# Optimization experiments

Measured on AMD Instinct MI355X. Metric: run time of the kernel, lower is better.

Reference implementation:

```python
import jax, jax.numpy as jnp
import numpy as np

N_NODES = 100000
N_EDGES = 1600000
N_GRAPHS = 1000
HID = 64
NEG_SLOPE = 0.2


def _glorot(key, shape):
    fan_in, fan_out = shape[0], shape[-1]
    lim = float(np.sqrt(6.0 / (fan_in + fan_out)))
    return jax.random.uniform(key, shape, jnp.float32, -lim, lim)


def setup_inputs() -> dict:
    key = jax.random.key(0)
    ks = jax.random.split(key, 20)
    x = jax.random.normal(ks[0], (N_NODES, 1), jnp.float32)
    edge_index = jax.random.randint(ks[1], (2, N_EDGES), 0, N_NODES, jnp.int64)
    batch = jnp.sort(jax.random.randint(ks[2], (N_NODES,), 0, N_GRAPHS, jnp.int64))
    inp = {"x": x, "edge_index": edge_index, "batch": batch}
    # GATv2Conv layer 1 (in=3 -> out=HID, 1 head)
    inp["Wl1"] = _glorot(ks[3], (3, HID)); inp["bl1"] = jnp.zeros((HID,), jnp.float32)
    inp["Wr1"] = _glorot(ks[4], (3, HID)); inp["br1"] = jnp.zeros((HID,), jnp.float32)
    inp["a1"] = _glorot(ks[5], (HID, 1))[:, 0]; inp["b1"] = jnp.zeros((HID,), jnp.float32)
    # GATv2Conv layer 2 (HID -> HID)
    inp["Wl2"] = _glorot(ks[6], (HID, HID)); inp["bl2"] = jnp.zeros((HID,), jnp.float32)
    inp["Wr2"] = _glorot(ks[7], (HID, HID)); inp["br2"] = jnp.zeros((HID,), jnp.float32)
    inp["a2"] = _glorot(ks[8], (HID, 1))[:, 0]; inp["b2"] = jnp.zeros((HID,), jnp.float32)
    # lin2 (HID -> 2)
    inp["W3"] = _glorot(ks[9], (HID, 2)); inp["b3"] = jnp.zeros((2,), jnp.float32)
    return inp


def gatv2_layer(x, src, dst, Wl, bl, Wr, br, a, b):
    """GATv2Conv, 1 head, add_self_loops=True, negative_slope=0.2."""
    n = x.shape[0]
    xl = x @ Wl + bl  # source-side transform [N, C]
    xr = x @ Wr + br  # target-side transform [N, C]
    loops = jnp.arange(n, dtype=src.dtype)
    s = jnp.concatenate([src, loops])
    d = jnp.concatenate([dst, loops])
    # per-edge attention logit: a^T LeakyReLU(xl[j] + xr[i])
    e = jax.nn.leaky_relu(xl[s] + xr[d], NEG_SLOPE) @ a  # [E+N]
    # segment softmax over incoming edges of each dst node
    m = jax.ops.segment_max(e, d, num_segments=n)
    ex = jnp.exp(e - m[d])
    denom = jax.ops.segment_sum(ex, d, num_segments=n)
    alpha = ex / denom[d]
    out = jax.ops.segment_sum(alpha[:, None] * xl[s], d, num_segments=n)
    return out + b


def reference(x, edge_index, batch, Wl1, bl1, Wr1, br1, a1, b1,
              Wl2, bl2, Wr2, br2, a2, b2, W3, b3):
    n = x.shape[0]
    src, dst = edge_index[0], edge_index[1]
    ones = jnp.ones((src.shape[0],), jnp.float32)
    deg_in = jax.ops.segment_sum(ones, dst, num_segments=n)   # bincount(dst)
    deg_out = jax.ops.segment_sum(ones, src, num_segments=n)  # bincount(src)
    h = jnp.concatenate([x, deg_in[:, None], deg_out[:, None]], axis=1)  # [N,3]
    h = gatv2_layer(h, src, dst, Wl1, bl1, Wr1, br1, a1, b1)
    h = jnp.tanh(h)
    h = gatv2_layer(h, src, dst, Wl2, bl2, Wr2, br2, a2, b2)
    # global_max_pool over graphs
    g = jax.ops.segment_max(h, batch, num_segments=N_GRAPHS)  # [G, HID]
    return g @ W3 + b3  # [G, 2]
```

## Files before the change

### kernel.cpp

```cpp
#include <hip/hip_runtime.h>
#include <hip/hip_bf16.h>
#include <hip/hip_fp16.h>

#define HID 64
#define NEG_SLOPE 0.2f
#define BLK_E 4096
#define EDGE_CAP 6144
#define NDB 16

typedef _Float16 f16x2 __attribute__((ext_vector_type(2)));


__global__ void k_hist2(const int* __restrict__ src, const int* __restrict__ dst,
                        int* __restrict__ histS, int* __restrict__ histD,
                        int E, int NB, int NBLK) {
    __shared__ int hs[512], hd[512];
    int t = threadIdx.x, blk = blockIdx.x;
    for (int b = t; b < NB; b += 1024) { hs[b] = 0; hd[b] = 0; }
    __syncthreads();
    int base = blk * BLK_E;
    #pragma unroll
    for (int k = 0; k < BLK_E / 1024; ++k) {
        int i = base + k * 1024 + t;
        if (i < E) {
            atomicAdd(&hs[src[i] >> 8], 1);
            atomicAdd(&hd[dst[i] >> 8], 1);
        }
    }
    __syncthreads();
    for (int b = t; b < NB; b += 1024) {
        histS[b * NBLK + blk] = hs[b];
        histD[b * NBLK + blk] = hd[b];
    }
}

__global__ void k_binscan(int* __restrict__ histS, int* __restrict__ histD,
                          int* __restrict__ totS, int* __restrict__ totD,
                          int NB, int NBLK) {
    __shared__ int s[512];
    int b = blockIdx.x;
    int* hist = histS; int* tot = totS;
    if (b >= NB) { b -= NB; hist = histD; tot = totD; }
    int t = threadIdx.x;
    int v = (t < NBLK) ? hist[b * NBLK + t] : 0;
    s[t] = v;
    __syncthreads();
    for (int o = 1; o < 512; o <<= 1) {
        int u = (t >= o) ? s[t - o] : 0;
        __syncthreads();
        s[t] += u;
        __syncthreads();
    }
    if (t < NBLK) hist[b * NBLK + t] = s[t] - v;
    if (t == 511) tot[b] = s[511];
}

__global__ void k_binoffset(const int* __restrict__ totS, const int* __restrict__ totD,
                            int* __restrict__ bsS, int* __restrict__ bsD,
                            int NB, int E, int* __restrict__ row_off, int N) {
    __shared__ int s[512];
    int t = threadIdx.x;
    int v = (t < NB) ? totS[t] : 0;
    s[t] = v; __syncthreads();
    for (int o = 1; o < 512; o <<= 1) {
        int u = (t >= o) ? s[t - o] : 0;
        __syncthreads(); s[t] += u; __syncthreads();
    }
    if (t < NB) bsS[t] = s[t] - v;
    if (t == 0) bsS[NB] = E;
    __syncthreads();
    v = (t < NB) ? totD[t] : 0;
    s[t] = v; __syncthreads();
    for (int o = 1; o < 512; o <<= 1) {
        int u = (t >= o) ? s[t - o] : 0;
        __syncthreads(); s[t] += u; __syncthreads();
    }
    if (t < NB) bsD[t] = s[t] - v;
    if (t == 0) { bsD[NB] = E; row_off[N] = E; }
}

__global__ void k_scatter_bins(const int* __restrict__ src, const int* __restrict__ dst,
                               const int* __restrict__ histS, const int* __restrict__ histD,
                               const int* __restrict__ bsS, const int* __restrict__ bsD,
                               unsigned* __restrict__ packS, unsigned* __restrict__ packD,
                               int E, int NB, int NBLK) {
    __shared__ int baseS[512], baseD[512];
    int t = threadIdx.x, blk = blockIdx.x;
    for (int b = t; b < NB; b += 1024) {
        baseS[b] = bsS[b] + histS[b * NBLK + blk];
        baseD[b] = bsD[b] + histD[b * NBLK + blk];
    }
    __syncthreads();
    int base = blk * BLK_E;
    #pragma unroll
    for (int k = 0; k < BLK_E / 1024; ++k) {
        int i = base + k * 1024 + t;
        if (i < E) {
            int sv = src[i], dv = dst[i];
            int pD = atomicAdd(&baseD[dv >> 8], 1);
            packD[pD] = ((unsigned)(dv & 255) << 24) | (unsigned)sv;
            int pS = atomicAdd(&baseS[sv >> 8], 1);
            packS[pS] = (unsigned)(sv & 255);
        }
    }
}

__global__ void k_csr_bin_fused(const unsigned* __restrict__ packD, const int* __restrict__ bsD,
                                const unsigned* __restrict__ packS, const int* __restrict__ bsS,
                                int* __restrict__ row_off, float* __restrict__ deg_in,
                                int* __restrict__ csr_src,
                                const float* __restrict__ x,
                                const float* __restrict__ Wl, const float* __restrict__ bl,
                                const float* __restrict__ Wr, const float* __restrict__ br,
                                __half* __restrict__ A, __half* __restrict__ B, int N) {
    __shared__ int cnt[256], off[256], cur[256], cntS[256];
    __shared__ unsigned eb[EDGE_CAP];
    int b = blockIdx.x, t = threadIdx.x;
    int lo = bsD[b], hi = bsD[b + 1], ne = hi - lo;
    bool fits = (ne <= EDGE_CAP);
    if (t < 256) { cnt[t] = 0; cntS[t] = 0; }
    __syncthreads();
    for (int i = t; i < ne; i += 1024) {
        unsigned v = packD[lo + i];
        if (fits) eb[i] = v;
        atomicAdd(&cnt[v >> 24], 1);
    }
    int loS = bsS[b], hiS = bsS[b + 1];
    for (int i = loS + t; i < hiS; i += 1024) atomicAdd(&cntS[packS[i] & 255], 1);
    __syncthreads();
    if (t < 256) off[t] = cnt[t];
    __syncthreads();
    for (int o = 1; o < 256; o <<= 1) {
        int u = 0;
        if (t < 256 && t >= o) u = off[t - o];
        __syncthreads();
        if (t < 256) off[t] += u;
        __syncthreads();
    }
    if (t < 256) {
        int ex = off[t] - cnt[t];
        cur[t] = lo + ex;
        int node = b * 256 + t;
        if (node < N) {
            row_off[node] = lo + ex;
            deg_in[node] = (float)cnt[t];
        }
    }
    __syncthreads();
    for (int i = t; i < ne; i += 1024) {
        unsigned v = fits ? eb[i] : packD[lo + i];
        int pos = atomicAdd(&cur[v >> 24], 1);
        csr_src[pos] = (int)(v & 0xFFFFFFu);
    }
    int nd = b * 256 + (t >> 2);
    if (nd < N) {
        float h0 = x[nd];
        float h1 = (float)cnt[t >> 2];
        float h2 = (float)cntS[t >> 2];
        int c0 = (t & 3) * 16;
        unsigned ua[4], ub[4];
        #pragma unroll
        for (int p = 0; p < 2; ++p) {
            #pragma unroll
            for (int q = 0; q < 4; ++q) {
                int c = c0 + p * 8 + q * 2;
                float a0 = h0 * Wl[c]     + h1 * Wl[64 + c]     + h2 * Wl[128 + c]     + bl[c];
                float a1 = h0 * Wl[c + 1] + h1 * Wl[64 + c + 1] + h2 * Wl[128 + c + 1] + bl[c + 1];
                float b0 = h0 * Wr[c]     + h1 * Wr[64 + c]     + h2 * Wr[128 + c]     + br[c];
                float b1 = h0 * Wr[c + 1] + h1 * Wr[64 + c + 1] + h2 * Wr[128 + c + 1] + br[c + 1];
                f16x2 pa; pa.x = (_Float16)a0; pa.y = (_Float16)a1;
                f16x2 pb; pb.x = (_Float16)b0; pb.y = (_Float16)b1;
                if (q < 4) { ua[q] = __builtin_bit_cast(unsigned, pa); ub[q] = __builtin_bit_cast(unsigned, pb); }
            }
            uint4 sa = make_uint4(ua[0], ua[1], ua[2], ua[3]);
            uint4 sb = make_uint4(ub[0], ub[1], ub[2], ub[3]);
            ((uint4*)A)[(size_t)nd * 8 + (t & 3) * 2 + p] = sa;
            ((uint4*)B)[(size_t)nd * 8 + (t & 3) * 2 + p] = sb;
        }
    }
}


__global__ void k_deghist(const float* __restrict__ deg_in, int* __restrict__ dhist, int N) {
    __shared__ int h[64];
    int t = threadIdx.x, b = blockIdx.x;
    if (t < 64) h[t] = 0;
    __syncthreads();
    int chunk = (N + NDB - 1) / NDB;
    int lo = b * chunk, hi = lo + chunk; if (hi > N) hi = N;
    for (int i = lo + t; i < hi; i += 1024) {
        int dg = (int)deg_in[i]; if (dg > 63) dg = 63;
        atomicAdd(&h[dg], 1);
    }
    __syncthreads();
    if (t < 64) dhist[t * NDB + b] = h[t];
}

__global__ void k_degscan(int* __restrict__ dhist) {
    __shared__ int s[1024];
    int t = threadIdx.x;
    int v = dhist[t];
    s[t] = v; __syncthreads();
    for (int o = 1; o < 1024; o <<= 1) {
        int u = (t >= o) ? s[t - o] : 0;
        __syncthreads(); s[t] += u; __syncthreads();
    }
    dhist[t] = s[t] - v;
}

__global__ void k_degscatter(const float* __restrict__ deg_in, const int* __restrict__ dhist,
                             int* __restrict__ perm, int N) {
    __shared__ int cur[64];
    int t = threadIdx.x, b = blockIdx.x;
    if (t < 64) cur[t] = dhist[t * NDB + b];
    __syncthreads();
    int chunk = (N + NDB - 1) / NDB;
    int lo = b * chunk, hi = lo + chunk; if (hi > N) hi = N;
    for (int i = lo + t; i < hi; i += 1024) {
        int dg = (int)deg_in[i]; if (dg > 63) dg = 63;
        int p = atomicAdd(&cur[dg], 1);
        perm[p] = i;
    }
}


struct H4 { f16x2 h[4]; };

__device__ __forceinline__ f16x2 bch2(unsigned u) {
    return __builtin_bit_cast(f16x2, u);
}

__device__ __forceinline__ H4 ld4(const uint4* __restrict__ T, size_t idx) {
    uint4 r = T[idx];
    H4 o;
    o.h[0] = bch2(r.x); o.h[1] = bch2(r.y); o.h[2] = bch2(r.z); o.h[3] = bch2(r.w);
    return o;
}

__device__ __forceinline__ float logit8(const H4& a, const H4& x,
                                        const float* __restrict__ awf, f16x2 ns2) {
    float t = 0.0f;
    #pragma unroll
    for (int j = 0; j < 4; ++j) {
        f16x2 s = a.h[j] + x.h[j];
        f16x2 l = __builtin_elementwise_max(s, ns2 * s);
        t = fmaf((float)l.x, awf[2 * j], t);
        t = fmaf((float)l.y, awf[2 * j + 1], t);
    }
    return t;
}

__device__ __forceinline__ void accum8(float* __restrict__ acc, const H4& a, float w) {
    #pragma unroll
    for (int j = 0; j < 4; ++j) {
        acc[2 * j]     = fmaf((float)a.h[j].x, w, acc[2 * j]);
        acc[2 * j + 1] = fmaf((float)a.h[j].y, w, acc[2 * j + 1]);
    }
}

template <typename OUT, bool TANH>
__global__ void k_gat_fused(const int* __restrict__ csr_src, const int* __restrict__ row_off,
                            const int* __restrict__ perm,
                            const __half* __restrict__ Ah, const __half* __restrict__ Bh,
                            const float* __restrict__ aw, const float* __restrict__ bias,
                            OUT* __restrict__ out, int N) {
    int tid = blockIdx.x * blockDim.x + threadIdx.x;
    int r = tid >> 3;
    int gl = threadIdx.x & 7;
    if (r >= N) return;
    int d = perm[N - 1 - r];

    const uint4* A16 = (const uint4*)Ah;
    const uint4* B16 = (const uint4*)Bh;
    f16x2 ns2;
    ns2.x = (_Float16)NEG_SLOPE; ns2.y = (_Float16)NEG_SLOPE;

    float awf[8], bw[8];
    {
        const float4* a4 = (const float4*)aw;
        const float4* b4 = (const float4*)bias;
        #pragma unroll
        for (int j = 0; j < 2; ++j) {
            float4 v = a4[gl * 2 + j];
            awf[4 * j] = v.x; awf[4 * j + 1] = v.y; awf[4 * j + 2] = v.z; awf[4 * j + 3] = v.w;
            float4 u = b4[gl * 2 + j];
            bw[4 * j] = u.x; bw[4 * j + 1] = u.y; bw[4 * j + 2] = u.z; bw[4 * j + 3] = u.w;
        }
    }

    size_t rowbase = (size_t)d * 8 + gl;
    H4 xh = ld4(B16, rowbase);
    H4 as = ld4(A16, rowbase);

    float t = logit8(as, xh, awf, ns2);
    t += __shfl_xor(t, 1); t += __shfl_xor(t, 2); t += __shfl_xor(t, 4);
    float m = t, denom = 1.0f;
    float acc[8];
    #pragma unroll
    for (int j = 0; j < 4; ++j) {
        acc[2 * j] = (float)as.h[j].x;
        acc[2 * j + 1] = (float)as.h[j].y;
    }

    int lo = row_off[d], hi = row_off[d + 1];
    int k = lo;
    for (; k + 3 < hi; k += 4) {
        int s0 = csr_src[k], s1 = csr_src[k + 1], s2 = csr_src[k + 2], s3 = csr_src[k + 3];
        H4 a0 = ld4(A16, (size_t)s0 * 8 + gl);
        H4 a1 = ld4(A16, (size_t)s1 * 8 + gl);
        H4 a2 = ld4(A16, (size_t)s2 * 8 + gl);
        H4 a3 = ld4(A16, (size_t)s3 * 8 + gl);
        float t0 = logit8(a0, xh, awf, ns2);
        float t1 = logit8(a1, xh, awf, ns2);
        float t2 = logit8(a2, xh, awf, ns2);
        float t3 = logit8(a3, xh, awf, ns2);
        t0 += __shfl_xor(t0, 1); t1 += __shfl_xor(t1, 1);
        t2 += __shfl_xor(t2, 1); t3 += __shfl_xor(t3, 1);
        t0 += __shfl_xor(t0, 2); t1 += __shfl_xor(t1, 2);
        t2 += __shfl_xor(t2, 2); t3 += __shfl_xor(t3, 2);
        t0 += __shfl_xor(t0, 4); t1 += __shfl_xor(t1, 4);
        t2 += __shfl_xor(t2, 4); t3 += __shfl_xor(t3, 4);
        float mx = fmaxf(fmaxf(t0, t1), fmaxf(t2, t3));
        if (mx > m) {
            float sc = __expf(m - mx);
            denom *= sc;
            #pragma unroll
            for (int j = 0; j < 8; ++j) acc[j] *= sc;
            m = mx;
        }
        float w0 = __expf(t0 - m), w1 = __expf(t1 - m);
        float w2 = __expf(t2 - m), w3 = __expf(t3 - m);
        denom += (w0 + w1) + (w2 + w3);
        accum8(acc, a0, w0);
        accum8(acc, a1, w1);
        accum8(acc, a2, w2);
        accum8(acc, a3, w3);
    }
    for (; k < hi; ++k) {
        int s0 = csr_src[k];
        H4 a0 = ld4(A16, (size_t)s0 * 8 + gl);
        float t0 = logit8(a0, xh, awf, ns2);
        t0 += __shfl_xor(t0, 1); t0 += __shfl_xor(t0, 2); t0 += __shfl_xor(t0, 4);
        if (t0 > m) {
            float sc = __expf(m - t0);
            denom *= sc;
            #pragma unroll
            for (int j = 0; j < 8; ++j) acc[j] *= sc;
            m = t0;
        }
        float w0 = __expf(t0 - m);
        denom += w0;
        accum8(acc, a0, w0);
    }

    float inv = 1.0f / denom;
    float v[8];
    #pragma unroll
    for (int j = 0; j < 8; ++j) {
        v[j] = acc[j] * inv + bw[j];
        if (TANH) v[j] = tanhf(v[j]);
    }
    if constexpr (sizeof(OUT) == 2) {
        unsigned u[4];
        #pragma unroll
        for (int j = 0; j < 4; ++j) {
            f16x2 p; p.x = (_Float16)v[2 * j]; p.y = (_Float16)v[2 * j + 1];
            u[j] = __builtin_bit_cast(unsigned, p);
        }
        ((uint4*)out)[(size_t)d * 8 + gl] = make_uint4(u[0], u[1], u[2], u[3]);
    } else {
        float4* o4 = (float4*)out;
        o4[(size_t)d * 16 + gl * 2]     = make_float4(v[0], v[1], v[2], v[3]);
        o4[(size_t)d * 16 + gl * 2 + 1] = make_float4(v[4], v[5], v[6], v[7]);
    }
}

__global__ __launch_bounds__(512) void k_xfrm2(
        const __half* __restrict__ H,
        const float* __restrict__ Wl, const float* __restrict__ bl,
        const float* __restrict__ Wr, const float* __restrict__ br,
        __half* __restrict__ A, __half* __restrict__ B, int N) {
    __shared__ float wls[4096];
    __shared__ float wrs[4096];
    __shared__ float hst[64 * 66];
    int t = threadIdx.x;
    int base = blockIdx.x * 64;

    ((float4*)wls)[t * 2]     = ((const float4*)Wl)[t * 2];
    ((float4*)wls)[t * 2 + 1] = ((const float4*)Wl)[t * 2 + 1];
    ((float4*)wrs)[t * 2]     = ((const float4*)Wr)[t * 2];
    ((float4*)wrs)[t * 2 + 1] = ((const float4*)Wr)[t * 2 + 1];

    {
        int nd = t >> 3, q = t & 7;
        int node = base + nd;
        uint4 hv = (node < N) ? ((const uint4*)H)[(size_t)node * 8 + q]
                              : make_uint4(0, 0, 0, 0);
        f16x2 p0 = bch2(hv.x), p1 = bch2(hv.y), p2 = bch2(hv.z), p3 = bch2(hv.w);
        int c = q * 8;
        hst[(c + 0) * 66 + nd] = (float)p0.x;
        hst[(c + 1) * 66 + nd] = (float)p0.y;
        hst[(c + 2) * 66 + nd] = (float)p1.x;
        hst[(c + 3) * 66 + nd] = (float)p1.y;
        hst[(c + 4) * 66 + nd] = (float)p2.x;
        hst[(c + 5) * 66 + nd] = (float)p2.y;
        hst[(c + 6) * 66 + nd] = (float)p3.x;
        hst[(c + 7) * 66 + nd] = (float)p3.y;
    }
    __syncthreads();

    int w = t >> 6, l = t & 63;
    float acL[8] = {0, 0, 0, 0, 0, 0, 0, 0};
    float acR[8] = {0, 0, 0, 0, 0, 0, 0, 0};
    #pragma unroll 4
    for (int kk = 0; kk < 64; ++kk) {
        float hv = hst[kk * 66 + l];
        const float4* wl4 = (const float4*)&wls[kk * 64 + w * 8];
        const float4* wr4 = (const float4*)&wrs[kk * 64 + w * 8];
        float4 w0 = wl4[0], w1 = wl4[1];
        float4 r0 = wr4[0], r1 = wr4[1];
        acL[0] = fmaf(hv, w0.x, acL[0]); acL[1] = fmaf(hv, w0.y, acL[1]);
        acL[2] = fmaf(hv, w0.z, acL[2]); acL[3] = fmaf(hv, w0.w, acL[3]);
        acL[4] = fmaf(hv, w1.x, acL[4]); acL[5] = fmaf(hv, w1.y, acL[5]);
        acL[6] = fmaf(hv, w1.z, acL[6]); acL[7] = fmaf(hv, w1.w, acL[7]);
        acR[0] = fmaf(hv, r0.x, acR[0]); acR[1] = fmaf(hv, r0.y, acR[1]);
        acR[2] = fmaf(hv, r0.z, acR[2]); acR[3] = fmaf(hv, r0.w, acR[3]);
        acR[4] = fmaf(hv, r1.x, acR[4]); acR[5] = fmaf(hv, r1.y, acR[5]);
        acR[6] = fmaf(hv, r1.z, acR[6]); acR[7] = fmaf(hv, r1.w, acR[7]);
    }

    int node = base + l;
    if (node < N) {
        float4 bl0 = ((const float4*)bl)[w * 2], bl1 = ((const float4*)bl)[w * 2 + 1];
        float4 br0 = ((const float4*)br)[w * 2], br1 = ((const float4*)br)[w * 2 + 1];
        __half2* A2 = (__half2*)A;
        __half2* B2 = (__half2*)B;
        size_t bo = (size_t)node * 32 + w * 4;
        A2[bo + 0] = __floats2half2_rn(acL[0] + bl0.x, acL[1] + bl0.y);
        A2[bo + 1] = __floats2half2_rn(acL[2] + bl0.z, acL[3] + bl0.w);
        A2[bo + 2] = __floats2half2_rn(acL[4] + bl1.x, acL[5] + bl1.y);
        A2[bo + 3] = __floats2half2_rn(acL[6] + bl1.z, acL[7] + bl1.w);
        B2[bo + 0] = __floats2half2_rn(acR[0] + br0.x, acR[1] + br0.y);
        B2[bo + 1] = __floats2half2_rn(acR[2] + br0.z, acR[3] + br0.w);
        B2[bo + 2] = __floats2half2_rn(acR[4] + br1.x, acR[5] + br1.y);
        B2[bo + 3] = __floats2half2_rn(acR[6] + br1.z, acR[7] + br1.w);
    }
}

__global__ void k_pool_final(const float* __restrict__ C, const float* __restrict__ b2,
                             const int* __restrict__ batch,
                             const float* __restrict__ W3, const float* __restrict__ b3,
                             float* __restrict__ out, int N, int G) {
    int w = (int)((blockIdx.x * (size_t)blockDim.x + threadIdx.x) >> 6);
    int lane = threadIdx.x & 63;
    if (w >= G) return;
    int lo = 0, hi = N;
    while (lo < hi) { int mid = (lo + hi) >> 1; if (batch[mid] < w) lo = mid + 1; else hi = mid; }
    int s0 = lo;
    hi = N;
    while (lo < hi) { int mid = (lo + hi) >> 1; if (batch[mid] < w + 1) lo = mid + 1; else hi = mid; }
    int e0 = lo;

    float acc = -INFINITY;
    int i = s0;
    for (; i + 3 < e0; i += 4) {
        float v0 = C[(size_t)i * HID + lane];
        float v1 = C[(size_t)(i + 1) * HID + lane];
        float v2 = C[(size_t)(i + 2) * HID + lane];
        float v3 = C[(size_t)(i + 3) * HID + lane];
        acc = fmaxf(acc, fmaxf(fmaxf(v0, v1), fmaxf(v2, v3)));
    }
    for (; i < e0; ++i) acc = fmaxf(acc, C[(size_t)i * HID + lane]);
    float v = acc + b2[lane];

    float p0 = v * W3[lane * 2];
    float p1 = v * W3[lane * 2 + 1];
    #pragma unroll
    for (int o = 32; o; o >>= 1) { p0 += __shfl_xor(p0, o); p1 += __shfl_xor(p1, o); }
    if (lane == 0) {
        out[(size_t)w * 2]     = p0 + b3[0];
        out[(size_t)w * 2 + 1] = p1 + b3[1];
    }
}

extern "C" void kernel_launch(void* const* d_in, const int* in_sizes, int n_in,
                              void* d_out, int out_size, void* d_ws, size_t ws_size,
                              hipStream_t stream) {
    const float* x     = (const float*)d_in[0];
    const int*   ei    = (const int*)d_in[1];
    const int*   batch = (const int*)d_in[2];
    const float* Wl1 = (const float*)d_in[3];
    const float* bl1 = (const float*)d_in[4];
    const float* Wr1 = (const float*)d_in[5];
    const float* br1 = (const float*)d_in[6];
    const float* a1  = (const float*)d_in[7];
    const float* b1  = (const float*)d_in[8];
    const float* Wl2 = (const float*)d_in[9];
    const float* bl2 = (const float*)d_in[10];
    const float* Wr2 = (const float*)d_in[11];
    const float* br2 = (const float*)d_in[12];
    const float* a2  = (const float*)d_in[13];
    const float* b2  = (const float*)d_in[14];
    const float* W3  = (const float*)d_in[15];
    const float* b3  = (const float*)d_in[16];

    const int N = in_sizes[0];
    const int E = in_sizes[1] / 2;
    const int G = out_size / 2;
    const int NB = (N + 255) >> 8;
    const int NBLK = (E + BLK_E - 1) / BLK_E;

    float* ws = (float*)d_ws;
    size_t off = 0;
    float*  C  = ws + off; off += (size_t)N * HID;
    __half* Ah = (__half*)(ws + off); off += (size_t)N * HID / 2;
    __half* Bh = (__half*)(ws + off); off += (size_t)N * HID / 2;
    int*   row_off = (int*)(ws + off); off += N + 1;
    int*   csr_src = (int*)(ws + off); off += E;
    float* deg_in  = ws + off; off += N;
    int*   perm    = (int*)(ws + off); off += N;
    int*   dhist   = (int*)(ws + off); off += 1024;
    int*   bsS  = (int*)(ws + off); off += NB + 1;
    int*   bsD  = (int*)(ws + off); off += NB + 1;
    int*   totS = (int*)(ws + off); off += NB;
    int*   totD = (int*)(ws + off); off += NB;

    unsigned* packD = (unsigned*)C;
    unsigned* packS = packD + E;
    int* histS = (int*)(packS + E);
    int* histD = histS + (size_t)NB * NBLK;
    __half* Chalf = (__half*)C;

    const int* src  = ei;
    const int* dstp = ei + E;

    const int BT = 256;
    dim3 blk(BT);
    int grid_g8 = (int)(((size_t)N * 8 + BT - 1) / BT);
    int grid_x2 = (N + 63) / 64;

    k_hist2<<<NBLK, 1024, 0, stream>>>(src, dstp, histS, histD, E, NB, NBLK);
    k_binscan<<<2 * NB, 512, 0, stream>>>(histS, histD, totS, totD, NB, NBLK);
    k_binoffset<<<1, 512, 0, stream>>>(totS, totD, bsS, bsD, NB, E, row_off, N);
    k_scatter_bins<<<NBLK, 1024, 0, stream>>>(src, dstp, histS, histD, bsS, bsD,
                                              packS, packD, E, NB, NBLK);
    k_csr_bin_fused<<<NB, 1024, 0, stream>>>(packD, bsD, packS, bsS, row_off, deg_in,
                                             csr_src, x, Wl1, bl1, Wr1, br1, Ah, Bh, N);

    k_deghist<<<NDB, 1024, 0, stream>>>(deg_in, dhist, N);
    k_degscan<<<1, 1024, 0, stream>>>(dhist);
    k_degscatter<<<NDB, 1024, 0, stream>>>(deg_in, dhist, perm, N);

    k_gat_fused<__half, true><<<grid_g8, blk, 0, stream>>>(csr_src, row_off, perm,
                                                           Ah, Bh, a1, b1, Chalf, N);

    k_xfrm2<<<grid_x2, 512, 0, stream>>>(Chalf, Wl2, bl2, Wr2, br2, Ah, Bh, N);
    k_gat_fused<float, false><<<grid_g8, blk, 0, stream>>>(csr_src, row_off, perm,
                                                           Ah, Bh, a2, b2, C, N);

    k_pool_final<<<(G * 64 + BT - 1) / BT, blk, 0, stream>>>(C, b2, batch, W3, b3,
                                                             (float*)d_out, N, G);
}
```

Measured before the change: 218.1 us.

## Restructure layer-2 transform to one node per thread with register-held features

The layer-2 node transform now assigns one node per thread. Each thread loads its 64-wide half feature row straight into registers instead of transposing it through shared memory, then computes 16 output columns at a time over 8 column blocks. Weights in shared memory are read with wave-uniform broadcast addresses, and the block shrinks to 128 threads. This removes the shared-memory transpose and its bank traffic, but it adds heavy register pressure (64 features plus 16 accumulators), gives each thread strided per-node global loads, and leaves fewer total threads. A redundant always-true guard in the layer-1 packing loop is also dropped.

Result: slower. 225.0 us (+3.1%).

```diff
diff --git a/kernel.cpp b/kernel.cpp
--- a/kernel.cpp
+++ b/kernel.cpp
@@ -170,7 +170,8 @@
                 float b1 = h0 * Wr[c + 1] + h1 * Wr[64 + c + 1] + h2 * Wr[128 + c + 1] + br[c + 1];
                 f16x2 pa; pa.x = (_Float16)a0; pa.y = (_Float16)a1;
                 f16x2 pb; pb.x = (_Float16)b0; pb.y = (_Float16)b1;
-                if (q < 4) { ua[q] = __builtin_bit_cast(unsigned, pa); ub[q] = __builtin_bit_cast(unsigned, pb); }
+                ua[q] = __builtin_bit_cast(unsigned, pa);
+                ub[q] = __builtin_bit_cast(unsigned, pb);
             }
             uint4 sa = make_uint4(ua[0], ua[1], ua[2], ua[3]);
             uint4 sb = make_uint4(ub[0], ub[1], ub[2], ub[3]);
@@ -375,75 +376,73 @@
     }
 }
 
-__global__ __launch_bounds__(512) void k_xfrm2(
+__global__ __launch_bounds__(128) void k_xfrm2(
         const __half* __restrict__ H,
         const float* __restrict__ Wl, const float* __restrict__ bl,
         const float* __restrict__ Wr, const float* __restrict__ br,
         __half* __restrict__ A, __half* __restrict__ B, int N) {
     __shared__ float wls[4096];
     __shared__ float wrs[4096];
-    __shared__ float hst[64 * 66];
+    __shared__ float bls[64], brs[64];
     int t = threadIdx.x;
-    int base = blockIdx.x * 64;
-
-    ((float4*)wls)[t * 2]     = ((const float4*)Wl)[t * 2];
-    ((float4*)wls)[t * 2 + 1] = ((const float4*)Wl)[t * 2 + 1];
-    ((float4*)wrs)[t * 2]     = ((const float4*)Wr)[t * 2];
-    ((float4*)wrs)[t * 2 + 1] = ((const float4*)Wr)[t * 2 + 1];
-
+
+    #pragma unroll
+    for (int u = 0; u < 8; ++u) {
+        ((float4*)wls)[t + 128 * u] = ((const float4*)Wl)[t + 128 * u];
+        ((float4*)wrs)[t + 128 * u] = ((const float4*)Wr)[t + 128 * u];
+    }
+    if (t < 64) { bls[t] = bl[t]; brs[t] = br[t]; }
+    __syncthreads();
+
+    int node = blockIdx.x * 128 + t;
+    if (node >= N) return;
+
+    float hf[64];
     {
-        int nd = t >> 3, q = t & 7;
-        int node = base + nd;
-        uint4 hv = (node < N) ? ((const uint4*)H)[(size_t)node * 8 + q]
-                              : make_uint4(0, 0, 0, 0);
-        f16x2 p0 = bch2(hv.x), p1 = bch2(hv.y), p2 = bch2(hv.z), p3 = bch2(hv.w);
-        int c = q * 8;
-        hst[(c + 0) * 66 + nd] = (float)p0.x;
-        hst[(c + 1) * 66 + nd] = (float)p0.y;
-        hst[(c + 2) * 66 + nd] = (float)p1.x;
-        hst[(c + 3) * 66 + nd] = (float)p1.y;
-        hst[(c + 4) * 66 + nd] = (float)p2.x;
-        hst[(c + 5) * 66 + nd] = (float)p2.y;
-        hst[(c + 6) * 66 + nd] = (float)p3.x;
-        hst[(c + 7) * 66 + nd] = (float)p3.y;
-    }
-    __syncthreads();
-
-    int w = t >> 6, l = t & 63;
-    float acL[8] = {0, 0, 0, 0, 0, 0, 0, 0};
-    float acR[8] = {0, 0, 0, 0, 0, 0, 0, 0};
-    #pragma unroll 4
-    for (int kk = 0; kk < 64; ++kk) {
-        float hv = hst[kk * 66 + l];
-        const float4* wl4 = (const float4*)&wls[kk * 64 + w * 8];
-        const float4* wr4 = (const float4*)&wrs[kk * 64 + w * 8];
-        float4 w0 = wl4[0], w1 = wl4[1];
-        float4 r0 = wr4[0], r1 = wr4[1];
-        acL[0] = fmaf(hv, w0.x, acL[0]); acL[1] = fmaf(hv, w0.y, acL[1]);
-        acL[2] = fmaf(hv, w0.z, acL[2]); acL[3] = fmaf(hv, w0.w, acL[3]);
-        acL[4] = fmaf(hv, w1.x, acL[4]); acL[5] = fmaf(hv, w1.y, acL[5]);
-        acL[6] = fmaf(hv, w1.z, acL[6]); acL[7] = fmaf(hv, w1.w, acL[7]);
-        acR[0] = fmaf(hv, r0.x, acR[0]); acR[1] = fmaf(hv, r0.y, acR[1]);
-        acR[2] = fmaf(hv, r0.z, acR[2]); acR[3] = fmaf(hv, r0.w, acR[3]);
-        acR[4] = fmaf(hv, r1.x, acR[4]); acR[5] = fmaf(hv, r1.y, acR[5]);
-        acR[6] = fmaf(hv, r1.z, acR[6]); acR[7] = fmaf(hv, r1.w, acR[7]);
-    }
-
-    int node = base + l;
-    if (node < N) {
-        float4 bl0 = ((const float4*)bl)[w * 2], bl1 = ((const float4*)bl)[w * 2 + 1];
-        float4 br0 = ((const float4*)br)[w * 2], br1 = ((const float4*)br)[w * 2 + 1];
-        __half2* A2 = (__half2*)A;
-        __half2* B2 = (__half2*)B;
-        size_t bo = (size_t)node * 32 + w * 4;
-        A2[bo + 0] = __floats2half2_rn(acL[0] + bl0.x, acL[1] + bl0.y);
-        A2[bo + 1] = __floats2half2_rn(acL[2] + bl0.z, acL[3] + bl0.w);
-        A2[bo + 2] = __floats2half2_rn(acL[4] + bl1.x, acL[5] + bl1.y);
-        A2[bo + 3] = __floats2half2_rn(acL[6] + bl1.z, acL[7] + bl1.w);
-        B2[bo + 0] = __floats2half2_rn(acR[0] + br0.x, acR[1] + br0.y);
-        B2[bo + 1] = __floats2half2_rn(acR[2] + br0.z, acR[3] + br0.w);
-        B2[bo + 2] = __floats2half2_rn(acR[4] + br1.x, acR[5] + br1.y);
-        B2[bo + 3] = __floats2half2_rn(acR[6] + br1.z, acR[7] + br1.w);
+        const uint4* Hp = (const uint4*)(H + (size_t)node * HID);
+        #pragma unroll
+        for (int q = 0; q < 8; ++q) {
+            uint4 rv = Hp[q];
+            f16x2 p0 = bch2(rv.x), p1 = bch2(rv.y), p2 = bch2(rv.z), p3 = bch2(rv.w);
+            hf[q * 8 + 0] = (float)p0.x; hf[q * 8 + 1] = (float)p0.y;
+            hf[q * 8 + 2] = (float)p1.x; hf[q * 8 + 3] = (float)p1.y;
+            hf[q * 8 + 4] = (float)p2.x; hf[q * 8 + 5] = (float)p2.y;
+            hf[q * 8 + 6] = (float)p3.x; hf[q * 8 + 7] = (float)p3.y;
+        }
+    }
+
+    #pragma unroll 1
+    for (int cb = 0; cb < 8; ++cb) {
+        const float* W  = (cb < 4) ? wls : wrs;
+        const float* bb = (cb < 4) ? bls : brs;
+        __half* OT      = (cb < 4) ? A : B;
+        int c0 = (cb & 3) * 16;
+        float acc[16] = {0, 0, 0, 0, 0, 0, 0, 0, 0, 0, 0, 0, 0, 0, 0, 0};
+        #pragma unroll
+        for (int kk = 0; kk < 64; ++kk) {
+            float hv = hf[kk];
+            const float4* wp = (const float4*)&W[kk * 64 + c0];
+            float4 w0 = wp[0], w1 = wp[1], w2 = wp[2], w3 = wp[3];
+            acc[0]  = fmaf(hv, w0.x, acc[0]);  acc[1]  = fmaf(hv, w0.y, acc[1]);
+            acc[2]  = fmaf(hv, w0.z, acc[2]);  acc[3]  = fmaf(hv, w0.w, acc[3]);
+            acc[4]  = fmaf(hv, w1.x, acc[4]);  acc[5]  = fmaf(hv, w1.y, acc[5]);
+            acc[6]  = fmaf(hv, w1.z, acc[6]);  acc[7]  = fmaf(hv, w1.w, acc[7]);
+            acc[8]  = fmaf(hv, w2.x, acc[8]);  acc[9]  = fmaf(hv, w2.y, acc[9]);
+            acc[10] = fmaf(hv, w2.z, acc[10]); acc[11] = fmaf(hv, w2.w, acc[11]);
+            acc[12] = fmaf(hv, w3.x, acc[12]); acc[13] = fmaf(hv, w3.y, acc[13]);
+            acc[14] = fmaf(hv, w3.z, acc[14]); acc[15] = fmaf(hv, w3.w, acc[15]);
+        }
+        unsigned u[8];
+        #pragma unroll
+        for (int j = 0; j < 8; ++j) {
+            f16x2 p;
+            p.x = (_Float16)(acc[2 * j]     + bb[c0 + 2 * j]);
+            p.y = (_Float16)(acc[2 * j + 1] + bb[c0 + 2 * j + 1]);
+            u[j] = __builtin_bit_cast(unsigned, p);
+        }
+        uint4* op = (uint4*)(OT + (size_t)node * HID + c0);
+        op[0] = make_uint4(u[0], u[1], u[2], u[3]);
+        op[1] = make_uint4(u[4], u[5], u[6], u[7]);
     }
 }
 
@@ -537,7 +536,7 @@
     const int BT = 256;
     dim3 blk(BT);
     int grid_g8 = (int)(((size_t)N * 8 + BT - 1) / BT);
-    int grid_x2 = (N + 63) / 64;
+    int grid_x2 = (N + 127) / 128;
 
     k_hist2<<<NBLK, 1024, 0, stream>>>(src, dstp, histS, histD, E, NB, NBLK);
     k_binscan<<<2 * NB, 512, 0, stream>>>(histS, histD, totS, totD, NB, NBLK);
@@ -554,7 +553,7 @@
     k_gat_fused<__half, true><<<grid_g8, blk, 0, stream>>>(csr_src, row_off, perm,
                                                            Ah, Bh, a1, b1, Chalf, N);
 
-    k_xfrm2<<<grid_x2, 512, 0, stream>>>(Chalf, Wl2, bl2, Wr2, br2, Ah, Bh, N);
+    k_xfrm2<<<grid_x2, 128, 0, stream>>>(Chalf, Wl2, bl2, Wr2, br2, Ah, Bh, N);
     k_gat_fused<float, false><<<grid_g8, blk, 0, stream>>>(csr_src, row_off, perm,
                                                            Ah, Bh, a2, b2, C, N);
 
```
